# Kernel optimization log

Measured on AMD Instinct MI355X. Metric: run time of the kernel, lower is better.

The kernel has to match this reference:

```python
import jax, jax.numpy as jnp
import numpy as np

CAL_W, BF_W, PCP_W, CX_W = 1.0, 1.0, 0.5, 0.5
LIQ_SCALE, EPS = 1.0, 1e-6
BIG = 1e30


def setup_inputs() -> dict:
    n_mat, n_str, W = 32, 256, 4
    N = n_mat * n_str
    rng = np.random.default_rng(0)
    lm = np.tile(np.linspace(-0.5, 0.5, n_str, dtype=np.float32), n_mat)
    tenor = np.repeat(np.linspace(0.02, 2.0, n_mat, dtype=np.float32), n_str)
    cp = (rng.random(N) > 0.5).astype(np.float32)
    geometry = np.stack([lm, tenor, cp], axis=1)
    liquidity = rng.standard_normal((N, 4)).astype(np.float32)
    predicted_iv = (0.1 + 0.5 * rng.random((N, 1))).astype(np.float32)
    node_embeddings = rng.standard_normal((N, 256)).astype(np.float32)
    node = np.arange(N, dtype=np.int32).reshape(n_mat, n_str)
    src_s, dst_s = [], []
    for k in range(1, W + 1):  # strikes k apart within each maturity
        src_s.append(node[:, :-k].ravel()); dst_s.append(node[:, k:].ravel())
    edge_index_strike = np.stack([np.concatenate(src_s), np.concatenate(dst_s)])
    edge_index_maturity = np.stack([node[:-1].ravel(), node[1:].ravel()])
    return {
        'node_embeddings': jnp.asarray(node_embeddings),
        'predicted_iv': jnp.asarray(predicted_iv),
        'geometry': jnp.asarray(geometry),
        'liquidity': jnp.asarray(liquidity),
        'edge_index_strike': jnp.asarray(edge_index_strike),
        'edge_index_maturity': jnp.asarray(edge_index_maturity),
        'max_degree': 2 * W,
    }


def _padded_neighbors(edge_index, N, D):
    # CSR-style padded neighbor lists: row i = all undirected neighbors of i, -1 pad.
    src, dst = edge_index[0], edge_index[1]
    owners = jnp.concatenate([src, dst])
    nbrs = jnp.concatenate([dst, src])
    order = jnp.argsort(owners)  # jax sort is stable -> preserves [dst|src] order
    own_s, nbr_s = owners[order], nbrs[order]
    start = jnp.searchsorted(own_s, jnp.arange(N, dtype=own_s.dtype))
    rank = jnp.arange(own_s.shape[0], dtype=jnp.int32) - start[own_s].astype(jnp.int32)
    return jnp.full((N, D), -1, dtype=jnp.int32).at[own_s, rank].set(nbr_s.astype(jnp.int32))


def _forward(node_embeddings, predicted_iv, geometry, liquidity, edge_index_strike, edge_index_maturity, max_degree):
    lm, tenor, cp = geometry[:, 0], geometry[:, 1], geometry[:, 2]
    lw = jax.nn.sigmoid(liquidity[:, 3] * LIQ_SCALE)
    tv = predicted_iv[:, 0] ** 2 * jnp.maximum(tenor, EPS)  # total variance w = iv^2 * tau
    N = lm.shape[0]
    is_call = cp > 0.5

    # --- calendar arbitrage: total variance nondecreasing in tenor over maturity edges
    ms, md = edge_index_maturity[0], edge_index_maturity[1]
    cvalid = tenor[ms] < tenor[md] - EPS
    cviol = jax.nn.relu(tv[ms] - tv[md])
    cw = jnp.minimum(lw[ms], lw[md])
    ncal = cvalid.sum()
    calendar = jnp.where(ncal > 0, jnp.where(cvalid, cw * cviol, 0.0).sum() / jnp.maximum(ncal, 1), 0.0)

    # --- padded call-neighborhoods over strike edges, sorted by log-moneyness
    nbr = _padded_neighbors(edge_index_strike, N, max_degree)  # [N, D]
    nbr_safe = jnp.maximum(nbr, 0)
    nvalid = (nbr >= 0) & is_call[nbr_safe]
    key = jnp.where(nvalid, lm[nbr_safe], jnp.inf)  # invalid entries pushed to the end
    order = jnp.argsort(key, axis=1)
    ns = jnp.take_along_axis(nbr_safe, order, axis=1)
    vs = jnp.take_along_axis(nvalid, order, axis=1)
    n1, n2, n3 = ns[:, :-2], ns[:, 1:-1], ns[:, 2:]  # consecutive sorted triplets
    trip = vs[:, 2:] & is_call[:, None]  # triplet fully valid iff 3rd slot valid
    lm1, lm2, lm3 = lm[n1], lm[n2], lm[n3]
    denom = lm3 - lm1 + EPS
    alpha = (lm3 - lm2) / denom
    beta = (lm2 - lm1) / denom
    w_pair = lw[:, None] * lw[n2]
    tcount = trip.sum()

    # --- butterfly: interpolated total variance must not exceed the middle node's
    bviol = jax.nn.relu(alpha * tv[n1] + beta * tv[n3] - tv[n2])
    butterfly = jnp.where(tcount > 0, jnp.where(trip, w_pair * bviol, 0.0).sum() / jnp.maximum(tcount, 1), 0.0)

    # --- convexity on embedding norms
    en = jnp.linalg.norm(node_embeddings, axis=1)
    xviol = jax.nn.relu(en[n2] - (alpha * en[n1] + (1.0 - alpha) * en[n3]))
    convexity = jnp.where(tcount > 0, jnp.where(trip, w_pair * xviol, 0.0).sum() / jnp.maximum(tcount, 1), 0.0)

    # --- put-call parity: nearest put in (lm, tenor) per call, sum-sq embedding dist
    is_put = cp < 0.5
    dist = (lm[:, None] - lm[None, :]) ** 2 + (tenor[:, None] - tenor[None, :]) ** 2  # [N, N]
    dist = jnp.where(is_put[None, :], dist, BIG)
    best = jnp.argmin(dist, axis=1)
    emb_d = jnp.sum((node_embeddings - node_embeddings[best]) ** 2, axis=1)
    n_calls, n_puts = is_call.sum(), is_put.sum()
    pcp = jnp.where((n_calls > 0) & (n_puts > 0),
                    jnp.where(is_call, lw * lw[best] * emb_d, 0.0).sum() / jnp.maximum(n_calls, 1), 0.0)

    total = CAL_W * calendar + BF_W * butterfly + PCP_W * pcp + CX_W * convexity
    # order matches the module's dict: calendar, butterfly, put_call, convexity, total
    return jnp.stack([calendar, butterfly, pcp, convexity, total])


def reference(node_embeddings, predicted_iv, geometry, liquidity, edge_index_strike, edge_index_maturity, max_degree):
    return _forward(node_embeddings, predicted_iv, geometry, liquidity, edge_index_strike, edge_index_maturity, max_degree)
```

## Files before the change

### kernel.cpp

```cpp
#include <hip/hip_runtime.h>
#include <math.h>

#define EPS 1e-6f
#define DMAX 8
#define HALFW (DMAX / 2)
#define PREB 512
#define PCPB 512
#define SPLITY 32
#define TAG 0x5A7E0000u
typedef unsigned long long ull;

__device__ __forceinline__ float waveSumF(float v) {
    #pragma unroll
    for (int m = 1; m < 64; m <<= 1) v += __shfl_xor(v, m, 64);
    return v;
}
__device__ __forceinline__ int waveSumI(int v) {
    #pragma unroll
    for (int m = 1; m < 64; m <<= 1) v += __shfl_xor(v, m, 64);
    return v;
}
__device__ __forceinline__ ull waveMinKey(ull v) {
    #pragma unroll
    for (int m = 1; m < 64; m <<= 1) {
        ull o = __shfl_xor(v, m, 64);
        v = (o < v) ? o : v;
    }
    return v;
}
__device__ __forceinline__ float sigmoidf(float x) {
    return 1.0f / (1.0f + expf(-x));
}


__global__ void k_pre(const float* __restrict__ emb, const float* __restrict__ iv,
                      const float* __restrict__ geom, const float* __restrict__ liq,
                      const int* __restrict__ es, const int* __restrict__ em,
                      float* lwA, float* tvA, float* lmA, float* enA, int* cpA, int* nbr,
                      float* calPartF, int* calPartI, int* ncPart, int* npPart,
                      int* acc, ull* partialKey,
                      int N, int ED, int Es, int Em, int nIB, int chunk) {
    const int lane = threadIdx.x & 63;

    if ((int)blockIdx.x < PREB) {
        const int tid = blockIdx.x * 256 + threadIdx.x;
        const int gsz = PREB * 256;

        if (blockIdx.x == 0 && threadIdx.x < 16) acc[threadIdx.x] = 0;

        int ic = 0, ip = 0;
        for (int i = tid; i < N; i += gsz) {
            float lm = geom[3*i], ten = geom[3*i+1], cp = geom[3*i+2];
            lmA[i] = lm;
            int c = (cp > 0.5f) ? 1 : 0;
            ic += c; ip += (cp < 0.5f) ? 1 : 0;
            cpA[i] = c;
            lwA[i] = sigmoidf(liq[4*i+3]);
            float v = iv[i];
            tvA[i] = v * v * fmaxf(ten, EPS);
        }

        const int wid = tid >> 6, nw = gsz >> 6, ED4 = ED >> 2;
        for (int r = wid; r < N; r += nw) {
            const float4* row = (const float4*)(emb + (size_t)r * ED);
            float s = 0.f;
            for (int t = lane; t < ED4; t += 64) {
                float4 a = row[t];
                s += a.x*a.x + a.y*a.y + a.z*a.z + a.w*a.w;
            }
            s = waveSumF(s);
            if (lane == 0) enA[r] = sqrtf(s);
        }

        float c = 0.f; int n = 0;
        for (int e = tid; e < Em; e += gsz) {
            int s = em[e], d = em[Em + e];
            float ts = geom[3*s+1], td = geom[3*d+1];
            if (ts < td - EPS) {
                n++;
                float ivs = iv[s], ivd = iv[d];
                float tvs = ivs*ivs*fmaxf(ts, EPS), tvd = ivd*ivd*fmaxf(td, EPS);
                float lws = sigmoidf(liq[4*s+3]), lwd = sigmoidf(liq[4*d+3]);
                c += fminf(lws, lwd) * fmaxf(tvs - tvd, 0.f);
            }
        }
        for (int e = tid; e < Es; e += gsz) {
            int s = es[e], d = es[Es + e];
            int k = d - s;
            if (k >= 1 && k <= HALFW) {
                nbr[s * DMAX + (HALFW + k - 1)] = (int)(TAG | (unsigned)d);
                nbr[d * DMAX + (HALFW - k)]     = (int)(TAG | (unsigned)s);
            }
        }

        __shared__ float sf[4];
        __shared__ int si[4][3];
        c = waveSumF(c); n = waveSumI(n);
        int sc = waveSumI(ic), sp = waveSumI(ip);
        int w = threadIdx.x >> 6;
        if (lane == 0) { sf[w] = c; si[w][0] = n; si[w][1] = sc; si[w][2] = sp; }
        __syncthreads();
        if (threadIdx.x == 0) {
            calPartF[blockIdx.x] = sf[0]+sf[1]+sf[2]+sf[3];
            calPartI[blockIdx.x] = si[0][0]+si[1][0]+si[2][0]+si[3][0];
            ncPart[blockIdx.x]   = si[0][1]+si[1][1]+si[2][1]+si[3][1];
            npPart[blockIdx.x]   = si[0][2]+si[1][2]+si[2][2]+si[3][2];
        }
        return;
    }

    __shared__ float2 stile[256];
    int ab = blockIdx.x - PREB;
    int ib = ab % nIB, y = ab / nIB;
    int i  = ib * 256 + threadIdx.x;
    float lmi = 0.f, teni = 0.f;
    if (i < N) { lmi = geom[3*i]; teni = geom[3*i+1]; }
    int j0 = y * chunk;
    int j1 = min(j0 + chunk, N);
    float mind0 = INFINITY, mind1 = INFINITY, mind2 = INFINITY, mind3 = INFINITY;
    int   minj0 = 0, minj1 = 1, minj2 = 2, minj3 = 3;
    for (int t0 = j0; t0 < j1; t0 += 256) {
        __syncthreads();
        int jj = t0 + threadIdx.x;
        if (jj < N) {
            float cp = geom[3*jj+2];
            stile[threadIdx.x] = make_float2((cp < 0.5f) ? geom[3*jj] : 1e19f, geom[3*jj+1]);
        } else {
            stile[threadIdx.x] = make_float2(1e19f, 0.f);
        }
        __syncthreads();
        #pragma unroll 8
        for (int t = 0; t < 256; t += 4) {
            float2 p0 = stile[t], p1 = stile[t+1], p2 = stile[t+2], p3 = stile[t+3];
            float d0 = (lmi-p0.x)*(lmi-p0.x) + (teni-p0.y)*(teni-p0.y);
            float d1 = (lmi-p1.x)*(lmi-p1.x) + (teni-p1.y)*(teni-p1.y);
            float d2 = (lmi-p2.x)*(lmi-p2.x) + (teni-p2.y)*(teni-p2.y);
            float d3 = (lmi-p3.x)*(lmi-p3.x) + (teni-p3.y)*(teni-p3.y);
            if (d0 < mind0) { mind0 = d0; minj0 = t0 + t; }
            if (d1 < mind1) { mind1 = d1; minj1 = t0 + t + 1; }
            if (d2 < mind2) { mind2 = d2; minj2 = t0 + t + 2; }
            if (d3 < mind3) { mind3 = d3; minj3 = t0 + t + 3; }
        }
    }
    ull k0 = ((ull)__float_as_uint(mind0) << 32) | (unsigned)minj0;
    ull k1 = ((ull)__float_as_uint(mind1) << 32) | (unsigned)minj1;
    ull k2 = ((ull)__float_as_uint(mind2) << 32) | (unsigned)minj2;
    ull k3 = ((ull)__float_as_uint(mind3) << 32) | (unsigned)minj3;
    ull k = k0; if (k1 < k) k = k1; if (k2 < k) k = k2; if (k3 < k) k = k3;
    if (i < N) partialKey[(size_t)i * SPLITY + y] = k;
}

__global__ void k_post(const float* __restrict__ emb, const ull* __restrict__ partialKey,
                       const int* __restrict__ cpA, const float* __restrict__ lwA,
                       const float* __restrict__ tvA, const float* __restrict__ lmA,
                       const float* __restrict__ enA, const int* __restrict__ nbr,
                       const float* __restrict__ calPartF, const int* __restrict__ calPartI,
                       const int* __restrict__ ncPart, const int* __restrict__ npPart,
                       int* acc, float* out, int N, int ED) {
    float* accF = (float*)acc;
    __shared__ float sblk[4];
    __shared__ float sblk2[4];
    __shared__ int   sblkI[4];
    __shared__ int sticket;
    const int lane = threadIdx.x & 63;
    const int w    = threadIdx.x >> 6;

    if ((int)blockIdx.x < PCPB) {
        const int gw = (blockIdx.x * 256 + threadIdx.x) >> 6;
        const int nw = PCPB * 4;
        const int ED4 = ED >> 2;
        float wacc = 0.f;
        for (int i = gw; i < N; i += nw) {
            ull k = (lane < SPLITY) ? partialKey[(size_t)i * SPLITY + lane] : ~0ULL;
            k = waveMinKey(k);
            int b = (int)(k & 0xffffffffULL);
            if (cpA[i] && b >= 0 && b < N) {
                const float4* ri = (const float4*)(emb + (size_t)i * ED);
                const float4* rb = (const float4*)(emb + (size_t)b * ED);
                float s = 0.f;
                for (int t = lane; t < ED4; t += 64) {
                    float4 a = ri[t], c = rb[t];
                    float dx = a.x-c.x, dy = a.y-c.y, dz = a.z-c.z, dw = a.w-c.w;
                    s += dx*dx + dy*dy + dz*dz + dw*dw;
                }
                s = waveSumF(s);
                wacc += lwA[i] * lwA[b] * s;
            }
        }
        if (lane == 0) sblk[w] = wacc;
        __syncthreads();
        if (threadIdx.x == 0) {
            float tot = sblk[0]+sblk[1]+sblk[2]+sblk[3];
            if (tot != 0.f) atomicAdd(&accF[3], tot);
        }
    } else {
        int i = ((int)blockIdx.x - PCPB) * 256 + threadIdx.x;
        float bf = 0.f, cx = 0.f; int tc = 0;
        if (i < N) {
            int ids[DMAX]; float key[DMAX]; int mv = 0;
            for (int slot = 0; slot < DMAX; slot++) {
                unsigned v = (unsigned)nbr[i * DMAX + slot];
                if ((v & 0xFFFF0000u) == TAG) {
                    int nb = (int)(v & 0xFFFFu);
                    if (cpA[nb]) {
                        float kk = lmA[nb];
                        int p = mv++;
                        while (p > 0 && key[p-1] > kk) { key[p] = key[p-1]; ids[p] = ids[p-1]; p--; }
                        key[p] = kk; ids[p] = nb;
                    }
                }
            }
            if (cpA[i] && mv >= 3) {
                float lwi = lwA[i];
                for (int j = 0; j + 2 < mv; j++) {
                    int n1 = ids[j], n2 = ids[j+1], n3 = ids[j+2];
                    float lm1 = key[j], lm2 = key[j+1], lm3 = key[j+2];
                    float denom = lm3 - lm1 + EPS;
                    float alpha = (lm3 - lm2) / denom;
                    float beta  = (lm2 - lm1) / denom;
                    float bviol = fmaxf(alpha * tvA[n1] + beta * tvA[n3] - tvA[n2], 0.f);
                    float xviol = fmaxf(enA[n2] - (alpha * enA[n1] + (1.0f - alpha) * enA[n3]), 0.f);
                    float wgt = lwi * lwA[n2];
                    bf += wgt * bviol; cx += wgt * xviol; tc++;
                }
            }
        }
        bf = waveSumF(bf); cx = waveSumF(cx); tc = waveSumI(tc);
        if (lane == 0) { sblk[w] = bf; sblk2[w] = cx; sblkI[w] = tc; }
        __syncthreads();
        if (threadIdx.x == 0) {
            float b4 = sblk[0]+sblk[1]+sblk[2]+sblk[3];
            float c4 = sblk2[0]+sblk2[1]+sblk2[2]+sblk2[3];
            int   t4 = sblkI[0]+sblkI[1]+sblkI[2]+sblkI[3];
            if (b4 != 0.f) atomicAdd(&accF[1], b4);
            if (c4 != 0.f) atomicAdd(&accF[2], c4);
            if (t4) atomicAdd(&acc[5], t4);
        }
    }

    if (threadIdx.x == 0) {
        __threadfence();
        sticket = atomicAdd(&acc[9], 1);
    }
    __syncthreads();
    if (sticket == (int)gridDim.x - 1) {
        float cs = 0.f; int cc = 0, ncall = 0, nput = 0;
        for (int t = threadIdx.x; t < PREB; t += 256) {
            cs += calPartF[t]; cc += calPartI[t]; ncall += ncPart[t]; nput += npPart[t];
        }
        cs = waveSumF(cs); cc = waveSumI(cc); ncall = waveSumI(ncall); nput = waveSumI(nput);
        if (lane == 0) { sblk[w] = cs; sblkI[w] = cc; sblk2[w] = (float)ncall; ((int*)&sblk2[0])[0] = 0; }
        __shared__ float fcs[4]; __shared__ int fcc[4], fnc[4], fnp[4];
        if (lane == 0) { fcs[w] = cs; fcc[w] = cc; fnc[w] = ncall; fnp[w] = nput; }
        __syncthreads();
        if (threadIdx.x == 0) {
            float calSum = fcs[0]+fcs[1]+fcs[2]+fcs[3];
            int   calCnt = fcc[0]+fcc[1]+fcc[2]+fcc[3];
            int   nCalls = fnc[0]+fnc[1]+fnc[2]+fnc[3];
            int   nPuts  = fnp[0]+fnp[1]+fnp[2]+fnp[3];
            float bfSum  = atomicAdd(&accF[1], 0.f);
            float cxSum  = atomicAdd(&accF[2], 0.f);
            float pcpSum = atomicAdd(&accF[3], 0.f);
            int   tcount = atomicAdd(&acc[5], 0);
            float cal = (calCnt > 0) ? calSum / (float)max(calCnt, 1) : 0.f;
            float bf  = (tcount > 0) ? bfSum / (float)tcount : 0.f;
            float cx  = (tcount > 0) ? cxSum / (float)tcount : 0.f;
            float pcp = (nCalls > 0 && nPuts > 0) ? pcpSum / (float)max(nCalls, 1) : 0.f;
            out[0] = cal; out[1] = bf; out[2] = pcp; out[3] = cx;
            out[4] = cal + bf + 0.5f * pcp + 0.5f * cx;
        }
    }
}

extern "C" void kernel_launch(void* const* d_in, const int* in_sizes, int n_in,
                              void* d_out, int out_size, void* d_ws, size_t ws_size,
                              hipStream_t stream) {
    const float* emb  = (const float*)d_in[0];
    const float* iv   = (const float*)d_in[1];
    const float* geom = (const float*)d_in[2];
    const float* liq  = (const float*)d_in[3];
    const int*   es   = (const int*)d_in[4];
    const int*   em   = (const int*)d_in[5];

    const int N  = in_sizes[1];
    const int ED = in_sizes[0] / N;
    const int Es = in_sizes[4] / 2;
    const int Em = in_sizes[5] / 2;

    int*   acc      = (int*)d_ws;
    float* calPartF = (float*)d_ws + 16;
    int*   calPartI = (int*)d_ws + 16 + PREB;
    int*   ncPart   = calPartI + PREB;
    int*   npPart   = ncPart + PREB;
    float* lwA      = (float*)(npPart + PREB);
    float* tvA      = lwA + N;
    float* lmA      = tvA + N;
    float* enA      = lmA + N;
    int*   cpA      = (int*)(enA + N);
    int*   nbr      = cpA + N;
    size_t keyOffB  = ((size_t)((char*)(nbr + (size_t)DMAX * N) - (char*)d_ws) + 7) & ~(size_t)7;
    ull*   partialKey = (ull*)((char*)d_ws + keyOffB);

    const int nIB = (N + 255) / 256;
    int chunk = (N + SPLITY - 1) / SPLITY;
    chunk = ((chunk + 255) / 256) * 256;

    k_pre<<<PREB + nIB * SPLITY, 256, 0, stream>>>(
        emb, iv, geom, liq, es, em,
        lwA, tvA, lmA, enA, cpA, nbr,
        calPartF, calPartI, ncPart, npPart, acc, partialKey,
        N, ED, Es, Em, nIB, chunk);

    const int nBtf = (N + 255) / 256;
    k_post<<<PCPB + nBtf, 256, 0, stream>>>(
        emb, partialKey, cpA, lwA, tvA, lmA, enA, nbr,
        calPartF, calPartI, ncPart, npPart, acc, (float*)d_out, N, ED);
}
```

Before: 110.2 us.

## Pack nearest-put distance math into float2 vectors and use one wave per node

```diff
diff --git a/kernel.cpp b/kernel.cpp
--- a/kernel.cpp
+++ b/kernel.cpp
@@ -5,10 +5,10 @@
 #define DMAX 8
 #define HALFW (DMAX / 2)
 #define PREB 512
-#define PCPB 512
 #define SPLITY 32
 #define TAG 0x5A7E0000u
 typedef unsigned long long ull;
+typedef float v2f __attribute__((ext_vector_type(2)));
 
 __device__ __forceinline__ float waveSumF(float v) {
     #pragma unroll
@@ -109,12 +109,15 @@
         return;
     }
 
-    __shared__ float2 stile[256];
+    __shared__ v2f slm2[128];
+    __shared__ v2f sten2[128];
     int ab = blockIdx.x - PREB;
     int ib = ab % nIB, y = ab / nIB;
     int i  = ib * 256 + threadIdx.x;
     float lmi = 0.f, teni = 0.f;
     if (i < N) { lmi = geom[3*i]; teni = geom[3*i+1]; }
+    v2f lmi2;  lmi2.x = lmi;  lmi2.y = lmi;
+    v2f teni2; teni2.x = teni; teni2.y = teni;
     int j0 = y * chunk;
     int j1 = min(j0 + chunk, N);
     float mind0 = INFINITY, mind1 = INFINITY, mind2 = INFINITY, mind3 = INFINITY;
@@ -122,24 +125,28 @@
     for (int t0 = j0; t0 < j1; t0 += 256) {
         __syncthreads();
         int jj = t0 + threadIdx.x;
+        float plm = 1e19f, pten = 0.f;
         if (jj < N) {
             float cp = geom[3*jj+2];
-            stile[threadIdx.x] = make_float2((cp < 0.5f) ? geom[3*jj] : 1e19f, geom[3*jj+1]);
-        } else {
-            stile[threadIdx.x] = make_float2(1e19f, 0.f);
-        }
+            pten = geom[3*jj+1];
+            if (cp < 0.5f) plm = geom[3*jj];
+        }
+        ((float*)slm2)[threadIdx.x]  = plm;
+        ((float*)sten2)[threadIdx.x] = pten;
         __syncthreads();
         #pragma unroll 8
-        for (int t = 0; t < 256; t += 4) {
-            float2 p0 = stile[t], p1 = stile[t+1], p2 = stile[t+2], p3 = stile[t+3];
-            float d0 = (lmi-p0.x)*(lmi-p0.x) + (teni-p0.y)*(teni-p0.y);
-            float d1 = (lmi-p1.x)*(lmi-p1.x) + (teni-p1.y)*(teni-p1.y);
-            float d2 = (lmi-p2.x)*(lmi-p2.x) + (teni-p2.y)*(teni-p2.y);
-            float d3 = (lmi-p3.x)*(lmi-p3.x) + (teni-p3.y)*(teni-p3.y);
-            if (d0 < mind0) { mind0 = d0; minj0 = t0 + t; }
-            if (d1 < mind1) { mind1 = d1; minj1 = t0 + t + 1; }
-            if (d2 < mind2) { mind2 = d2; minj2 = t0 + t + 2; }
-            if (d3 < mind3) { mind3 = d3; minj3 = t0 + t + 3; }
+        for (int t = 0; t < 128; t += 2) {
+            v2f la = slm2[t],  lb = slm2[t+1];
+            v2f ta = sten2[t], tb = sten2[t+1];
+            v2f dla = lmi2 - la,  dlb = lmi2 - lb;
+            v2f dta = teni2 - ta, dtb = teni2 - tb;
+            v2f da = dla*dla + dta*dta;
+            v2f db = dlb*dlb + dtb*dtb;
+            int jb = t0 + 2*t;
+            if (da.x < mind0) { mind0 = da.x; minj0 = jb; }
+            if (da.y < mind1) { mind1 = da.y; minj1 = jb + 1; }
+            if (db.x < mind2) { mind2 = db.x; minj2 = jb + 2; }
+            if (db.y < mind3) { mind3 = db.y; minj3 = jb + 3; }
         }
     }
     ull k0 = ((ull)__float_as_uint(mind0) << 32) | (unsigned)minj0;
@@ -156,7 +163,7 @@
                        const float* __restrict__ enA, const int* __restrict__ nbr,
                        const float* __restrict__ calPartF, const int* __restrict__ calPartI,
                        const int* __restrict__ ncPart, const int* __restrict__ npPart,
-                       int* acc, float* out, int N, int ED) {
+                       int* acc, float* out, int N, int ED, int nPcp) {
     float* accF = (float*)acc;
     __shared__ float sblk[4];
     __shared__ float sblk2[4];
@@ -165,36 +172,33 @@
     const int lane = threadIdx.x & 63;
     const int w    = threadIdx.x >> 6;
 
-    if ((int)blockIdx.x < PCPB) {
-        const int gw = (blockIdx.x * 256 + threadIdx.x) >> 6;
-        const int nw = PCPB * 4;
+    if ((int)blockIdx.x < nPcp) {
+        const int i = (blockIdx.x * 256 + threadIdx.x) >> 6;
         const int ED4 = ED >> 2;
-        float wacc = 0.f;
-        for (int i = gw; i < N; i += nw) {
+        float contrib = 0.f;
+        if (i < N && cpA[i]) {
             ull k = (lane < SPLITY) ? partialKey[(size_t)i * SPLITY + lane] : ~0ULL;
             k = waveMinKey(k);
             int b = (int)(k & 0xffffffffULL);
-            if (cpA[i] && b >= 0 && b < N) {
-                const float4* ri = (const float4*)(emb + (size_t)i * ED);
-                const float4* rb = (const float4*)(emb + (size_t)b * ED);
-                float s = 0.f;
-                for (int t = lane; t < ED4; t += 64) {
-                    float4 a = ri[t], c = rb[t];
-                    float dx = a.x-c.x, dy = a.y-c.y, dz = a.z-c.z, dw = a.w-c.w;
-                    s += dx*dx + dy*dy + dz*dz + dw*dw;
-                }
-                s = waveSumF(s);
-                wacc += lwA[i] * lwA[b] * s;
-            }
-        }
-        if (lane == 0) sblk[w] = wacc;
+            const float4* ri = (const float4*)(emb + (size_t)i * ED);
+            const float4* rb = (const float4*)(emb + (size_t)b * ED);
+            float s = 0.f;
+            for (int t = lane; t < ED4; t += 64) {
+                float4 a = ri[t], c = rb[t];
+                float dx = a.x-c.x, dy = a.y-c.y, dz = a.z-c.z, dw = a.w-c.w;
+                s += dx*dx + dy*dy + dz*dz + dw*dw;
+            }
+            s = waveSumF(s);
+            contrib = lwA[i] * lwA[b] * s;
+        }
+        if (lane == 0) sblk[w] = contrib;
         __syncthreads();
         if (threadIdx.x == 0) {
             float tot = sblk[0]+sblk[1]+sblk[2]+sblk[3];
             if (tot != 0.f) atomicAdd(&accF[3], tot);
         }
     } else {
-        int i = ((int)blockIdx.x - PCPB) * 256 + threadIdx.x;
+        int i = ((int)blockIdx.x - nPcp) * 256 + threadIdx.x;
         float bf = 0.f, cx = 0.f; int tc = 0;
         if (i < N) {
             int ids[DMAX]; float key[DMAX]; int mv = 0;
@@ -249,7 +253,6 @@
             cs += calPartF[t]; cc += calPartI[t]; ncall += ncPart[t]; nput += npPart[t];
         }
         cs = waveSumF(cs); cc = waveSumI(cc); ncall = waveSumI(ncall); nput = waveSumI(nput);
-        if (lane == 0) { sblk[w] = cs; sblkI[w] = cc; sblk2[w] = (float)ncall; ((int*)&sblk2[0])[0] = 0; }
         __shared__ float fcs[4]; __shared__ int fcc[4], fnc[4], fnp[4];
         if (lane == 0) { fcs[w] = cs; fcc[w] = cc; fnc[w] = ncall; fnp[w] = nput; }
         __syncthreads();
@@ -311,8 +314,9 @@
         calPartF, calPartI, ncPart, npPart, acc, partialKey,
         N, ED, Es, Em, nIB, chunk);
 
+    const int nPcp = (N + 3) / 4;
     const int nBtf = (N + 255) / 256;
-    k_post<<<PCPB + nBtf, 256, 0, stream>>>(
+    k_post<<<nPcp + nBtf, 256, 0, stream>>>(
         emb, partialKey, cpA, lwA, tvA, lmA, enA, nbr,
-        calPartF, calPartI, ncPart, npPart, acc, (float*)d_out, N, ED);
-}
+        calPartF, calPartI, ncPart, npPart, acc, (float*)d_out, N, ED, nPcp);
+}
```

Result: slower. 148.1 us (+34.4%).
